# Kernel tuning notes

Hardware: AMD Instinct MI355X
Metric: run time of the kernel (lower is better)

## Reference

```python
import jax, jax.numpy as jnp
import numpy as np

B = 8192      # number of molecules (graphs)
T = 524288    # total flat candidates (avg 64 per graph, jagged)
D = 128       # embed_dim
V = 100000    # unique templates (table has V+1 rows incl. 'unknown')


def setup_inputs() -> dict:
    key = jax.random.key(0)
    k1, k2, k3 = jax.random.split(key, 3)
    rng = np.random.default_rng(0)
    # jagged lengths, each segment >= 1, summing exactly to T
    lengths = rng.multinomial(T - B, np.ones(B) / B) + 1
    seg_ids = np.repeat(np.arange(B), lengths)           # [T], sorted segment ids
    offsets = np.concatenate([[0], np.cumsum(lengths)[:-1]])
    target_pos = offsets + rng.integers(0, lengths)      # one target per segment
    return {
        "graph_embed": jax.random.normal(k1, (B, D), dtype=jnp.float32),
        "tpl_embedding": jax.random.normal(k2, (V + 1, D), dtype=jnp.float32),
        "cand_idx": jax.random.randint(k3, (T,), 0, V + 1),
        "seg_ids": jnp.asarray(seg_ids, dtype=jnp.int32),
        "target_pos": jnp.asarray(target_pos, dtype=jnp.int32),
    }


def reference(graph_embed, tpl_embedding, cand_idx, seg_ids, target_pos):
    num_seg = graph_embed.shape[0]
    # gather candidate (template) embeddings: [T, D]
    cand_embed = tpl_embedding[cand_idx]
    # gather graph embedding per candidate (torch.gather with rep_indices): [T, D]
    g = graph_embed[seg_ids]
    # inner-product attention score per candidate: [T]
    logits = jnp.sum(g * cand_embed, axis=1)
    # jagged (segment-wise) log-softmax over variable-length candidate lists
    seg_max = jax.ops.segment_max(logits, seg_ids, num_segments=num_seg)
    shifted = logits - seg_max[seg_ids]
    seg_sum = jax.ops.segment_sum(jnp.exp(shifted), seg_ids, num_segments=num_seg)
    log_prob = shifted - jnp.log(seg_sum)[seg_ids]
    # gather the log-prob of the target template per graph: [B]
    return log_prob[target_pos]
```

## Files before the change

### kernel.cpp

```cpp
#include <hip/hip_runtime.h>

#define D 128
#define LOG2E 1.4426950408889634f
#define LN2   0.6931471805599453f

__global__ void seg_bounds_kernel(const int* __restrict__ seg_ids,
                                  int* __restrict__ seg_start,
                                  int T, int B) {
    int t = blockIdx.x * blockDim.x + threadIdx.x;
    if (t >= T) return;
    if (t == 0) {
        seg_start[0] = 0;
    } else if (seg_ids[t] != seg_ids[t - 1]) {
        seg_start[seg_ids[t]] = t;
    }
    if (t == T - 1) seg_start[B] = T;
}

__global__ __launch_bounds__(256) void logits_kernel(
    const float* __restrict__ graph_embed,
    const float* __restrict__ tpl_embedding,
    const int* __restrict__ cand_idx,
    const int* __restrict__ seg_ids,
    float* __restrict__ logits,
    int T)
{
    const int sl  = threadIdx.x & 31;
    const int hw  = (blockIdx.x * blockDim.x + threadIdx.x) >> 5;
    const int nhw = (gridDim.x * blockDim.x) >> 5;

    for (int t0 = hw; t0 < T; t0 += 4 * nhw) {
        int  t[4];
        bool vld[4];
        #pragma unroll
        for (int j = 0; j < 4; ++j) {
            const int tj = t0 + j * nhw;
            vld[j] = (tj < T);
            t[j]   = vld[j] ? tj : t0;
        }

        int c[4], s[4];
        #pragma unroll
        for (int j = 0; j < 4; ++j) { c[j] = cand_idx[t[j]]; s[j] = seg_ids[t[j]]; }

        float4 x[4], g[4];
        #pragma unroll
        for (int j = 0; j < 4; ++j)
            x[j] = ((const float4*)(tpl_embedding + (size_t)c[j] * D))[sl];
        #pragma unroll
        for (int j = 0; j < 4; ++j)
            g[j] = ((const float4*)(graph_embed + (size_t)s[j] * D))[sl];

        float p[4];
        #pragma unroll
        for (int j = 0; j < 4; ++j)
            p[j] = fmaf(g[j].x, x[j].x,
                   fmaf(g[j].y, x[j].y,
                   fmaf(g[j].z, x[j].z, g[j].w * x[j].w)));

        #pragma unroll
        for (int off = 16; off >= 1; off >>= 1) {
            #pragma unroll
            for (int j = 0; j < 4; ++j)
                p[j] += __shfl_xor(p[j], off);
        }

        if (sl == 0) {
            #pragma unroll
            for (int j = 0; j < 4; ++j)
                if (vld[j]) logits[t[j]] = p[j];
        }
    }
}

__global__ __launch_bounds__(64) void seg_reduce_kernel(
    const float* __restrict__ logits,
    const int* __restrict__ seg_start,
    const int* __restrict__ target_pos,
    float* __restrict__ out)
{
    const int b    = blockIdx.x;
    const int lane = threadIdx.x;
    const int start = seg_start[b];
    const int end   = seg_start[b + 1];

    float m = -3.0e38f;
    float s = 0.0f;

    for (int t = start + lane; t < end; t += 64) {
        const float x = logits[t] * LOG2E;
        if (x <= m) {
            s += exp2f(x - m);
        } else {
            s = fmaf(s, exp2f(m - x), 1.0f);
            m = x;
        }
    }

    #pragma unroll
    for (int off = 32; off >= 1; off >>= 1) {
        const float m2 = __shfl_xor(m, off);
        const float s2 = __shfl_xor(s, off);
        const float M  = fmaxf(m, m2);
        s = s * exp2f(m - M) + s2 * exp2f(m2 - M);
        m = M;
    }

    if (lane == 0) {
        const float tl = logits[target_pos[b]] * LOG2E;
        out[b] = (tl - m - log2f(s)) * LN2;
    }
}

extern "C" void kernel_launch(void* const* d_in, const int* in_sizes, int n_in,
                              void* d_out, int out_size, void* d_ws, size_t ws_size,
                              hipStream_t stream) {
    const float* graph_embed   = (const float*)d_in[0];
    const float* tpl_embedding = (const float*)d_in[1];
    const int*   cand_idx      = (const int*)d_in[2];
    const int*   seg_ids       = (const int*)d_in[3];
    const int*   target_pos    = (const int*)d_in[4];
    float*       out           = (float*)d_out;

    const int B = in_sizes[0] / D;
    const int T = in_sizes[2];

    int*   seg_start = (int*)d_ws;
    float* logits    = (float*)d_ws + (((B + 1) + 63) & ~63);

    seg_bounds_kernel<<<(T + 255) / 256, 256, 0, stream>>>(seg_ids, seg_start, T, B);

    logits_kernel<<<2048, 256, 0, stream>>>(graph_embed, tpl_embedding,
                                            cand_idx, seg_ids, logits, T);

    seg_reduce_kernel<<<B, 64, 0, stream>>>(logits, seg_start, target_pos, out);
}
```

Baseline: 135.9 us.

## Convert template table to fp16 per call and gather half-precision rows

Adds a pass that converts the full template embedding table to fp16 in workspace each call. The logits kernel then gathers 8-byte half rows instead of 16-byte float rows, halving the gather traffic. The conversion itself reads and writes the whole table every call, which may offset the savings, and it lowers precision of the logits. The fallback fp32 kernel is also reduced to a 2-way unroll.

```diff
diff --git a/kernel.cpp b/kernel.cpp
--- a/kernel.cpp
+++ b/kernel.cpp
@@ -1,20 +1,95 @@
 #include <hip/hip_runtime.h>
+#include <hip/hip_fp16.h>
 
 #define D 128
 #define LOG2E 1.4426950408889634f
 #define LN2   0.6931471805599453f
+
+__global__ __launch_bounds__(256) void tpl_half_kernel(
+    const float4* __restrict__ src,
+    uint2* __restrict__ dst,
+    int n4)
+{
+    const int stride = gridDim.x * blockDim.x;
+    for (int i = blockIdx.x * blockDim.x + threadIdx.x; i < n4; i += stride) {
+        const float4 v = src[i];
+        const __half2 h01 = __float22half2_rn(make_float2(v.x, v.y));
+        const __half2 h23 = __float22half2_rn(make_float2(v.z, v.w));
+        uint2 o;
+        o.x = *reinterpret_cast<const unsigned*>(&h01);
+        o.y = *reinterpret_cast<const unsigned*>(&h23);
+        dst[i] = o;
+    }
+}
 
 __global__ void seg_bounds_kernel(const int* __restrict__ seg_ids,
                                   int* __restrict__ seg_start,
                                   int T, int B) {
     int t = blockIdx.x * blockDim.x + threadIdx.x;
     if (t >= T) return;
-    if (t == 0) {
-        seg_start[0] = 0;
-    } else if (seg_ids[t] != seg_ids[t - 1]) {
-        seg_start[seg_ids[t]] = t;
-    }
+    if (t == 0) seg_start[0] = 0;
+    else if (seg_ids[t] != seg_ids[t - 1]) seg_start[seg_ids[t]] = t;
     if (t == T - 1) seg_start[B] = T;
+}
+
+__global__ __launch_bounds__(256) void logits_half_kernel(
+    const float* __restrict__ graph_embed,
+    const __half* __restrict__ tpl_h,
+    const int* __restrict__ cand_idx,
+    const int* __restrict__ seg_ids,
+    float* __restrict__ logits,
+    int T)
+{
+    const int sl  = threadIdx.x & 31;
+    const int hw  = (blockIdx.x * blockDim.x + threadIdx.x) >> 5;
+    const int nhw = (gridDim.x * blockDim.x) >> 5;
+
+    for (int t0 = hw; t0 < T; t0 += 4 * nhw) {
+        int  t[4];
+        bool vld[4];
+        #pragma unroll
+        for (int j = 0; j < 4; ++j) {
+            const int tj = t0 + j * nhw;
+            vld[j] = (tj < T);
+            t[j]   = vld[j] ? tj : t0;
+        }
+
+        int c[4], s[4];
+        #pragma unroll
+        for (int j = 0; j < 4; ++j) { c[j] = cand_idx[t[j]]; s[j] = seg_ids[t[j]]; }
+
+        uint2  x[4];
+        float4 g[4];
+        #pragma unroll
+        for (int j = 0; j < 4; ++j)
+            x[j] = ((const uint2*)(tpl_h + (size_t)c[j] * D))[sl];
+        #pragma unroll
+        for (int j = 0; j < 4; ++j)
+            g[j] = ((const float4*)(graph_embed + (size_t)s[j] * D))[sl];
+
+        float p[4];
+        #pragma unroll
+        for (int j = 0; j < 4; ++j) {
+            const float2 f01 = __half22float2(*reinterpret_cast<const __half2*>(&x[j].x));
+            const float2 f23 = __half22float2(*reinterpret_cast<const __half2*>(&x[j].y));
+            p[j] = fmaf(g[j].x, f01.x,
+                   fmaf(g[j].y, f01.y,
+                   fmaf(g[j].z, f23.x, g[j].w * f23.y)));
+        }
+
+        #pragma unroll
+        for (int off = 16; off >= 1; off >>= 1) {
+            #pragma unroll
+            for (int j = 0; j < 4; ++j)
+                p[j] += __shfl_xor(p[j], off);
+        }
+
+        if (sl == 0) {
+            #pragma unroll
+            for (int j = 0; j < 4; ++j)
+                if (vld[j]) logits[t[j]] = p[j];
+        }
+    }
 }
 
 __global__ __launch_bounds__(256) void logits_kernel(
@@ -29,46 +104,30 @@
     const int hw  = (blockIdx.x * blockDim.x + threadIdx.x) >> 5;
     const int nhw = (gridDim.x * blockDim.x) >> 5;
 
-    for (int t0 = hw; t0 < T; t0 += 4 * nhw) {
-        int  t[4];
-        bool vld[4];
-        #pragma unroll
-        for (int j = 0; j < 4; ++j) {
-            const int tj = t0 + j * nhw;
-            vld[j] = (tj < T);
-            t[j]   = vld[j] ? tj : t0;
-        }
-
-        int c[4], s[4];
-        #pragma unroll
-        for (int j = 0; j < 4; ++j) { c[j] = cand_idx[t[j]]; s[j] = seg_ids[t[j]]; }
-
-        float4 x[4], g[4];
-        #pragma unroll
-        for (int j = 0; j < 4; ++j)
-            x[j] = ((const float4*)(tpl_embedding + (size_t)c[j] * D))[sl];
-        #pragma unroll
-        for (int j = 0; j < 4; ++j)
-            g[j] = ((const float4*)(graph_embed + (size_t)s[j] * D))[sl];
-
-        float p[4];
-        #pragma unroll
-        for (int j = 0; j < 4; ++j)
-            p[j] = fmaf(g[j].x, x[j].x,
-                   fmaf(g[j].y, x[j].y,
-                   fmaf(g[j].z, x[j].z, g[j].w * x[j].w)));
+    for (int t0 = hw; t0 < T; t0 += 2 * nhw) {
+        const int t1 = t0 + nhw;
+        const bool has1 = (t1 < T);
+        const int c0 = cand_idx[t0];
+        const int s0 = seg_ids[t0];
+        const int c1 = has1 ? cand_idx[t1] : c0;
+        const int s1 = has1 ? seg_ids[t1] : s0;
+
+        const float4 x0 = ((const float4*)(tpl_embedding + (size_t)c0 * D))[sl];
+        const float4 g0 = ((const float4*)(graph_embed   + (size_t)s0 * D))[sl];
+        const float4 x1 = ((const float4*)(tpl_embedding + (size_t)c1 * D))[sl];
+        const float4 g1 = ((const float4*)(graph_embed   + (size_t)s1 * D))[sl];
+
+        float p0 = fmaf(g0.x, x0.x, fmaf(g0.y, x0.y, fmaf(g0.z, x0.z, g0.w * x0.w)));
+        float p1 = fmaf(g1.x, x1.x, fmaf(g1.y, x1.y, fmaf(g1.z, x1.z, g1.w * x1.w)));
 
         #pragma unroll
         for (int off = 16; off >= 1; off >>= 1) {
-            #pragma unroll
-            for (int j = 0; j < 4; ++j)
-                p[j] += __shfl_xor(p[j], off);
-        }
-
+            p0 += __shfl_xor(p0, off);
+            p1 += __shfl_xor(p1, off);
+        }
         if (sl == 0) {
-            #pragma unroll
-            for (int j = 0; j < 4; ++j)
-                if (vld[j]) logits[t[j]] = p[j];
+            logits[t0] = p0;
+            if (has1) logits[t1] = p1;
         }
     }
 }
@@ -122,16 +181,31 @@
     const int*   target_pos    = (const int*)d_in[4];
     float*       out           = (float*)d_out;
 
-    const int B = in_sizes[0] / D;
-    const int T = in_sizes[2];
-
-    int*   seg_start = (int*)d_ws;
-    float* logits    = (float*)d_ws + (((B + 1) + 63) & ~63);
+    const int B  = in_sizes[0] / D;
+    const int VE = in_sizes[1];
+    const int T  = in_sizes[2];
+
+    size_t off = 0;
+    auto alloc = [&](size_t bytes) {
+        void* p = (char*)d_ws + off;
+        off += (bytes + 255) & ~(size_t)255;
+        return p;
+    };
+    int*    seg_start = (int*)   alloc((size_t)(B + 1) * 4);
+    float*  logits    = (float*) alloc((size_t)T * 4);
+    __half* tpl_h     = (__half*)alloc((size_t)VE * 2);
 
     seg_bounds_kernel<<<(T + 255) / 256, 256, 0, stream>>>(seg_ids, seg_start, T, B);
 
-    logits_kernel<<<2048, 256, 0, stream>>>(graph_embed, tpl_embedding,
-                                            cand_idx, seg_ids, logits, T);
+    if (off <= ws_size) {
+        tpl_half_kernel<<<2048, 256, 0, stream>>>((const float4*)tpl_embedding,
+                                                  (uint2*)tpl_h, VE / 4);
+        logits_half_kernel<<<2048, 256, 0, stream>>>(graph_embed, tpl_h,
+                                                     cand_idx, seg_ids, logits, T);
+    } else {
+        logits_kernel<<<2048, 256, 0, stream>>>(graph_embed, tpl_embedding,
+                                                cand_idx, seg_ids, logits, T);
+    }
 
     seg_reduce_kernel<<<B, 64, 0, stream>>>(logits, seg_start, target_pos, out);
 }
```

After: 133.3 us. No clear change (-1.9%).
